# Kernel tuning notes

Hardware: AMD Instinct MI355X
Metric: run time of the kernel (lower is better)

Reference implementation:

```python
import jax, jax.numpy as jnp
import numpy as np

N_INP = 256
N_OUT = 16
H = 1024
UH = 32  # uni_hidden_unit
BATCH = 16384


def setup_inputs() -> dict:
    key = jax.random.key(0)
    ks = jax.random.split(key, 16)
    s = 0.02
    return {
        "x": jax.random.normal(ks[0], (BATCH, N_INP), dtype=jnp.float32),
        # main MLP: n_inp -> 1024 -> 1024 -> n_out
        "W0": jax.random.normal(ks[1], (N_INP, H), dtype=jnp.float32) * s,
        "b0": jnp.zeros((H,), jnp.float32),
        "W1": jax.random.normal(ks[2], (H, H), dtype=jnp.float32) * s,
        "b1": jnp.zeros((H,), jnp.float32),
        "W2": jax.random.normal(ks[3], (H, N_OUT), dtype=jnp.float32) * s,
        "b2": jnp.zeros((N_OUT,), jnp.float32),
        # stacked per-feature uni MLPs: 1 -> UH -> UH -> n_out, one per feature
        "uw1": jax.random.normal(ks[4], (N_INP, UH), dtype=jnp.float32) * s,
        "ub1": jnp.zeros((N_INP, UH), jnp.float32),
        "uw2": jax.random.normal(ks[5], (N_INP, UH, UH), dtype=jnp.float32) * s,
        "ub2": jnp.zeros((N_INP, UH), jnp.float32),
        "uw3": jax.random.normal(ks[6], (N_INP, UH, N_OUT), dtype=jnp.float32) * s,
        "ub3": jnp.zeros((N_INP, N_OUT), jnp.float32),
    }


def reference(x, W0, b0, W1, b1, W2, b2, uw1, ub1, uw2, ub2, uw3, ub3):
    # main MLP: Linear+ReLU, Linear+ReLU, Linear
    y = jax.nn.relu(x @ W0 + b0)
    y = jax.nn.relu(y @ W1 + b1)
    y = y @ W2 + b2  # [B, n_out]

    # per-feature univariate MLPs, vectorized over the feature axis i
    # input to uni MLP i is x[:, i:i+1]  -> first Linear(1, UH)
    h = jax.nn.relu(x[:, :, None] * uw1[None] + ub1[None])       # [B, I, UH]
    h = jax.nn.relu(jnp.einsum('bif,ifo->bio', h, uw2) + ub2[None])  # [B, I, UH]
    u = jnp.einsum('bif,ifo->bio', h, uw3) + ub3[None]           # [B, I, n_out]
    return y + u.sum(axis=1)
```

## Files before the change

kernel.cpp:

```cpp
#include <hip/hip_runtime.h>

typedef unsigned short u16;
typedef __attribute__((ext_vector_type(4))) float f32x4;
typedef __attribute__((ext_vector_type(4))) int i32x4;
typedef __attribute__((ext_vector_type(8))) __bf16 bf16x8;
typedef __attribute__((ext_vector_type(4))) unsigned short u16x4;

#define BATCH 16384
#define NINP 256
#define HID 1024
#define NOUT 16

__device__ __forceinline__ u16 f2bf(float f) {
  unsigned u = __builtin_bit_cast(unsigned, f);
  u += 0x7FFFu + ((u >> 16) & 1u);
  return (u16)(u >> 16);
}
__device__ __forceinline__ f32x4 mfma_bb(bf16x8 a, bf16x8 b, f32x4 c) {
  return __builtin_amdgcn_mfma_f32_16x16x32_bf16(a, b, c, 0, 0, 0);
}
__device__ __forceinline__ void gload_lds16(const void* g, void* l) {
  __builtin_amdgcn_global_load_lds(
      (const __attribute__((address_space(1))) void*)g,
      (__attribute__((address_space(3))) void*)l, 16, 0, 0);
}

static const size_t OFF_H0   = 0;
static const size_t OFF_PART = 0;
static const size_t OFF_H1   = 33554432;
static const size_t OFF_XB   = 33554432;
static const size_t OFF_W0T  = 67108864;
static const size_t OFF_W1T  = 67633152;
static const size_t OFF_W2T  = 69730304;
static const size_t OFF_UWP  = 69763072;
static const size_t OFF_CB   = 70811648;

__global__ __launch_bounds__(256) void k_prep(
    const float* __restrict__ x,
    const float* __restrict__ W0, const float* __restrict__ W1,
    const float* __restrict__ W2,
    const float* __restrict__ uw1, const float* __restrict__ ub1,
    const float* __restrict__ uw2, const float* __restrict__ ub2,
    const float* __restrict__ uw3, const float* __restrict__ b2,
    const float* __restrict__ ub3,
    u16* __restrict__ xb,
    u16* __restrict__ W0T, u16* __restrict__ W1T, u16* __restrict__ W2T,
    char* __restrict__ uwp, float* __restrict__ cb)
{
  __shared__ float tile[32][33];
  const int bid = blockIdx.x;
  const int tid = threadIdx.x;

  if (bid < 1312) {
    const float* src; u16* dst; int K, N, kb, ob;
    if (bid < 256)       { src = W0; dst = W0T; K = 256;  N = 1024; int t = bid;        kb = (t & 7) * 32;  ob = (t >> 3) * 32; }
    else if (bid < 1280) { src = W1; dst = W1T; K = 1024; N = 1024; int t = bid - 256;  kb = (t & 31) * 32; ob = (t >> 5) * 32; }
    else                 { src = W2; dst = W2T; K = 1024; N = 16;   int t = bid - 1280; kb = t * 32;        ob = 0; }
    const int tx = tid & 31, ty = tid >> 5;
    for (int r = ty; r < 32; r += 8)
      if (ob + tx < N) tile[r][tx] = src[(size_t)(kb + r) * N + ob + tx];
    __syncthreads();
    for (int r = ty; r < 32; r += 8)
      if (ob + r < N) dst[(size_t)(ob + r) * K + kb + tx] = f2bf(tile[tx][r]);
  } else if (bid < 5408) {
    const int idx = ((bid - 1312) * 256 + tid) * 4;
    const float4 v = *(const float4*)&x[idx];
    u16x4 o4 = { f2bf(v.x), f2bf(v.y), f2bf(v.z), f2bf(v.w) };
    *(u16x4*)&xb[idx] = o4;
  } else if (bid < 5664) {
    const int e = ((bid - 5408) * 256 + tid) * 4;
    const float4 v = *(const float4*)&uw2[e];
    const int i = e >> 10, f = (e >> 5) & 31, o = e & 31;
    const float vv[4] = { v.x, v.y, v.z, v.w };
    u16* blob16 = (u16*)(uwp + (size_t)i * 4096);
#pragma unroll
    for (int d = 0; d < 4; ++d) {
      const int oo = o + d;
      const int lane = ((f >> 3) << 4) | (oo & 15);
      blob16[256 + (oo >> 4) * 512 + lane * 8 + (f & 7)] = f2bf(vv[d]);
    }
  } else if (bid < 5792) {
    const int e = ((bid - 5664) * 256 + tid) * 4;
    const float4 v = *(const float4*)&uw3[e];
    const int i = e >> 9, f = (e >> 4) & 31, o2 = e & 15;
    const int s = (f < 16) ? (((f >> 2) << 3) + (f & 3))
                           : ((((f - 16) >> 2) << 3) + 4 + (f & 3));
    const float vv[4] = { v.x, v.y, v.z, v.w };
    u16* blob16 = (u16*)(uwp + (size_t)i * 4096);
#pragma unroll
    for (int d = 0; d < 4; ++d)
      blob16[1280 + ((s >> 3) * 16 + o2 + d) * 8 + (s & 7)] = f2bf(vv[d]);
  } else if (bid < 5816) {
    const int e4 = (bid - 5792) * 256 + tid;
    const int i = e4 / 24, r4 = e4 % 24;
    const float* src = (r4 < 8)  ? &uw1[i * 32 + r4 * 4]
                     : (r4 < 16) ? &ub1[i * 32 + (r4 - 8) * 4]
                                 : &ub2[i * 32 + (r4 - 16) * 4];
    *(float4*)(uwp + (size_t)i * 4096 + r4 * 16) = *(const float4*)src;
  } else {
    __shared__ float red[16][16];
    const int ig = tid >> 4, o = tid & 15;
    float s = 0.f;
#pragma unroll
    for (int k = 0; k < 16; ++k) s += ub3[(ig * 16 + k) * 16 + o];
    red[ig][o] = s;
    __syncthreads();
    if (tid < 16) {
      float t = b2[tid];
#pragma unroll
      for (int k = 0; k < 16; ++k) t += red[k][tid];
      cb[tid] = t;
    }
  }
}

__global__ __launch_bounds__(512, 2) void k_gemm8(
    const u16* __restrict__ A, const u16* __restrict__ BT,
    const float* __restrict__ bias, u16* __restrict__ C,
    int M, int N, int K)
{
  extern __shared__ __align__(16) char lds[];
  const int tid = threadIdx.x;
  const int lane = tid & 63, wid = tid >> 6;
  const int l15 = lane & 15, g = lane >> 4;
  const int wA = wid >> 2;
  const int wn = wid & 3;
  const int nbn = N >> 8;
  int logical = blockIdx.x;
  { const int nwg = gridDim.x;
    if ((nwg & 7) == 0) { const int q = nwg >> 3; logical = (logical & 7) * q + (logical >> 3); } }
  const int bm = logical / nbn, bn = logical - bm * nbn;
  const size_t rb = (size_t)bm * 256, cb = (size_t)bn * 256;

  const int q7 = l15 & 7;
  const int arow0 = wA * 128 + l15;
  const int brow0 = wn * 64 + l15;

  char* const ldsA = lds;
  char* const ldsB = lds + 65536;

  const u16* Ag = A + rb * K;
  const u16* Bg = BT + cb * K;

  f32x4 acc[8][4] = {};
  const int NT = K >> 6;

#define STAGE(arr, src, ktE, s) do { \
    const int G_ = (s) * 512 + tid; \
    const int row_ = G_ >> 3; \
    const int c8_ = (G_ & 7) ^ (row_ & 7); \
    gload_lds16(&(src)[(size_t)row_ * K + (ktE) + c8_ * 8], (arr) + G_ * 16); \
  } while (0)

#define ARD(bp, m, kk) (*(const bf16x8*)((bp) + (((arow0 + (m) * 16) * 8 + (((kk) * 4 + g) ^ q7)) << 4)))
#define BRD(bp, n, kk) (*(const bf16x8*)((bp) + (((brow0 + (n) * 16) * 8 + (((kk) * 4 + g) ^ q7)) << 4)))

#pragma unroll
  for (int s = 0; s < 4; ++s) STAGE(ldsA, Ag, 0, s);
#pragma unroll
  for (int s = 0; s < 4; ++s) STAGE(ldsB, Bg, 0, s);
  asm volatile("s_waitcnt vmcnt(0)" ::: "memory");
  __builtin_amdgcn_s_barrier();

  for (int t = 0; t < NT; ++t) {
    const int b = t & 1;
    const char* Ab = ldsA + b * 32768;
    const char* Bb = ldsB + b * 32768;
    char* An = ldsA + (b ^ 1) * 32768;
    char* Bn = ldsB + (b ^ 1) * 32768;
    const int kt1 = (t + 1) << 6;
    const bool stg = (t + 1 < NT);
    bf16x8 av[4][2], bv0[2][2], bv1[2][2];

#pragma unroll
    for (int m = 0; m < 4; ++m) { av[m][0] = ARD(Ab, m, 0); av[m][1] = ARD(Ab, m, 1); }
#pragma unroll
    for (int n = 0; n < 2; ++n) { bv0[n][0] = BRD(Bb, n, 0); bv0[n][1] = BRD(Bb, n, 1); }
    if (stg) { STAGE(An, Ag, kt1, 0); STAGE(Bn, Bg, kt1, 0); }
    __builtin_amdgcn_s_barrier();
    __builtin_amdgcn_s_setprio(1);
#pragma unroll
    for (int m = 0; m < 4; ++m)
#pragma unroll
      for (int n = 0; n < 2; ++n) {
        acc[m][n] = mfma_bb(av[m][0], bv0[n][0], acc[m][n]);
        acc[m][n] = mfma_bb(av[m][1], bv0[n][1], acc[m][n]);
      }
    __builtin_amdgcn_s_setprio(0);
    __builtin_amdgcn_s_barrier();

#pragma unroll
    for (int n = 0; n < 2; ++n) { bv1[n][0] = BRD(Bb, n + 2, 0); bv1[n][1] = BRD(Bb, n + 2, 1); }
    if (stg) { STAGE(An, Ag, kt1, 1); STAGE(Bn, Bg, kt1, 1); STAGE(An, Ag, kt1, 2); }
    __builtin_amdgcn_s_barrier();
    __builtin_amdgcn_s_setprio(1);
#pragma unroll
    for (int m = 0; m < 4; ++m)
#pragma unroll
      for (int n = 0; n < 2; ++n) {
        acc[m][n + 2] = mfma_bb(av[m][0], bv1[n][0], acc[m][n + 2]);
        acc[m][n + 2] = mfma_bb(av[m][1], bv1[n][1], acc[m][n + 2]);
      }
    __builtin_amdgcn_s_setprio(0);
    __builtin_amdgcn_s_barrier();

#pragma unroll
    for (int m = 0; m < 4; ++m) { av[m][0] = ARD(Ab, m + 4, 0); av[m][1] = ARD(Ab, m + 4, 1); }
    if (stg) { STAGE(Bn, Bg, kt1, 2); STAGE(An, Ag, kt1, 3); STAGE(Bn, Bg, kt1, 3); }
    __builtin_amdgcn_s_barrier();
    __builtin_amdgcn_s_setprio(1);
#pragma unroll
    for (int m = 0; m < 4; ++m)
#pragma unroll
      for (int n = 0; n < 2; ++n) {
        acc[m + 4][n + 2] = mfma_bb(av[m][0], bv1[n][0], acc[m + 4][n + 2]);
        acc[m + 4][n + 2] = mfma_bb(av[m][1], bv1[n][1], acc[m + 4][n + 2]);
      }
    __builtin_amdgcn_s_setprio(0);
    __builtin_amdgcn_s_barrier();

    __builtin_amdgcn_s_setprio(1);
#pragma unroll
    for (int m = 0; m < 4; ++m)
#pragma unroll
      for (int n = 0; n < 2; ++n) {
        acc[m + 4][n] = mfma_bb(av[m][0], bv0[n][0], acc[m + 4][n]);
        acc[m + 4][n] = mfma_bb(av[m][1], bv0[n][1], acc[m + 4][n]);
      }
    __builtin_amdgcn_s_setprio(0);
    asm volatile("s_waitcnt vmcnt(0)" ::: "memory");
    __builtin_amdgcn_s_barrier();
  }
#undef STAGE
#undef ARD
#undef BRD

  const int colb = (int)cb + wn * 64;
  const int rowb = (int)rb + wA * 128;
#pragma unroll
  for (int n = 0; n < 4; ++n) {
    const int col = colb + n * 16 + l15;
    const float bvs = bias[col];
#pragma unroll
    for (int m = 0; m < 8; ++m)
#pragma unroll
      for (int r = 0; r < 4; ++r) {
        const int row = rowb + m * 16 + g * 4 + r;
        C[(size_t)row * N + col] = f2bf(fmaxf(acc[m][n][r] + bvs, 0.f));
      }
  }
}

__global__ __launch_bounds__(256, 4) void k_uni(
    const float* __restrict__ x,
    const char* __restrict__ uwp,
    const u16* __restrict__ H1, const u16* __restrict__ W2T,
    float* __restrict__ part)
{
  const int tid = threadIdx.x, lane = tid & 63, wid = tid >> 6;
  const int l15 = lane & 15, g = lane >> 4;
  const int chunk = blockIdx.x & 7, rowblk = blockIdx.x >> 3;
  const int rb_blk = rowblk * 128;
  const int rb = rb_blk + wid * 32;
  const int i0 = chunk * 32;

  __shared__ __align__(16) float xt[128][33];
  __shared__ __align__(16) char wbuf[2][4096];

  {
    const int r0 = tid >> 3, c4 = (tid & 7) << 2;
#pragma unroll
    for (int rr = 0; rr < 128; rr += 32)
      *(float4*)&xt[rr + r0][c4] =
          *(const float4*)&x[(size_t)(rb_blk + rr + r0) * NINP + i0 + c4];
  }
  gload_lds16(uwp + (size_t)i0 * 4096 + tid * 16, &wbuf[0][tid * 16]);
  __syncthreads();

  const f32x4 zero4 = {0.f, 0.f, 0.f, 0.f};
  f32x4 acc0 = zero4, acc1 = zero4;
  const float* xr0 = &xt[wid * 32 + l15][0];
  const float* xr1 = &xt[wid * 32 + 16 + l15][0];

#pragma unroll 2
  for (int ii = 0; ii < 32; ++ii) {
    const int nxt = (ii + 1) & 31;
    gload_lds16(uwp + (size_t)(i0 + nxt) * 4096 + tid * 16,
                &wbuf[(ii + 1) & 1][tid * 16]);

    const char* bp = &wbuf[ii & 1][0];
    const f32x4 w1lo = *(const f32x4*)(bp + g * 32);
    const f32x4 w1hi = *(const f32x4*)(bp + g * 32 + 16);
    const f32x4 b1lo = *(const f32x4*)(bp + 128 + g * 32);
    const f32x4 b1hi = *(const f32x4*)(bp + 128 + g * 32 + 16);
    const f32x4 bb0  = *(const f32x4*)(bp + 256 + g * 16);
    const f32x4 bb1  = *(const f32x4*)(bp + 320 + g * 16);
    const bf16x8 bv0 = *(const bf16x8*)(bp + 512 + lane * 16);
    const bf16x8 bv1 = *(const bf16x8*)(bp + 1536 + lane * 16);
    const bf16x8 b3  = *(const bf16x8*)(bp + 2560 + lane * 16);
    const float xv0 = xr0[ii], xv1 = xr1[ii];

    bf16x8 af0, af1;
#pragma unroll
    for (int j = 0; j < 4; ++j) {
      af0[j]     = (__bf16)fmaxf(fmaf(xv0, w1lo[j], b1lo[j]), 0.f);
      af0[4 + j] = (__bf16)fmaxf(fmaf(xv0, w1hi[j], b1hi[j]), 0.f);
      af1[j]     = (__bf16)fmaxf(fmaf(xv1, w1lo[j], b1lo[j]), 0.f);
      af1[4 + j] = (__bf16)fmaxf(fmaf(xv1, w1hi[j], b1hi[j]), 0.f);
    }

    const f32x4 d00 = mfma_bb(bv0, af0, bb0);
    const f32x4 d10 = mfma_bb(bv1, af0, bb1);
    const f32x4 d01 = mfma_bb(bv0, af1, bb0);
    const f32x4 d11 = mfma_bb(bv1, af1, bb1);

    bf16x8 h20, h21;
#pragma unroll
    for (int j = 0; j < 4; ++j) {
      h20[j]     = (__bf16)fmaxf(d00[j], 0.f);
      h20[4 + j] = (__bf16)fmaxf(d10[j], 0.f);
      h21[j]     = (__bf16)fmaxf(d01[j], 0.f);
      h21[4 + j] = (__bf16)fmaxf(d11[j], 0.f);
    }

    acc0 = mfma_bb(b3, h20, acc0);
    acc1 = mfma_bb(b3, h21, acc1);

    __syncthreads();
  }

  {
    const int kb0 = chunk * 128;
#pragma unroll
    for (int kk = 0; kk < 4; ++kk) {
      const int kb = kb0 + kk * 32;
      const bf16x8 a0 = __builtin_bit_cast(bf16x8,
          *(const i32x4*)&H1[(size_t)(rb + l15) * HID + kb + g * 8]);
      const bf16x8 a1 = __builtin_bit_cast(bf16x8,
          *(const i32x4*)&H1[(size_t)(rb + 16 + l15) * HID + kb + g * 8]);
      const bf16x8 bv = __builtin_bit_cast(bf16x8,
          *(const i32x4*)&W2T[l15 * HID + kb + g * 8]);
      acc0 = mfma_bb(bv, a0, acc0);
      acc1 = mfma_bb(bv, a1, acc1);
    }
  }

  float* p = part + ((size_t)chunk * BATCH + rb) * NOUT;
  *(f32x4*)&p[l15 * 16 + g * 4] = acc0;
  *(f32x4*)&p[(16 + l15) * 16 + g * 4] = acc1;
}

__global__ __launch_bounds__(256) void k_reduce(
    const float* __restrict__ part, const float* __restrict__ cb,
    float* __restrict__ out)
{
  const int j4 = blockIdx.x * 256 + threadIdx.x;
  const float4 c = ((const float4*)cb)[j4 & 3];
  const float4* p = (const float4*)part;
  float rx = c.x, ry = c.y, rz = c.z, rw = c.w;
#pragma unroll
  for (int cc = 0; cc < 8; ++cc) {
    const float4 a = p[cc * 65536 + j4];
    rx += a.x; ry += a.y; rz += a.z; rw += a.w;
  }
  float4 r; r.x = rx; r.y = ry; r.z = rz; r.w = rw;
  ((float4*)out)[j4] = r;
}

extern "C" void kernel_launch(void* const* d_in, const int* in_sizes, int n_in,
                              void* d_out, int out_size, void* d_ws, size_t ws_size,
                              hipStream_t stream) {
  (void)in_sizes; (void)n_in; (void)out_size; (void)ws_size;
  const float* x   = (const float*)d_in[0];
  const float* W0  = (const float*)d_in[1];
  const float* b0  = (const float*)d_in[2];
  const float* W1  = (const float*)d_in[3];
  const float* b1  = (const float*)d_in[4];
  const float* W2  = (const float*)d_in[5];
  const float* b2  = (const float*)d_in[6];
  const float* uw1 = (const float*)d_in[7];
  const float* ub1 = (const float*)d_in[8];
  const float* uw2 = (const float*)d_in[9];
  const float* ub2 = (const float*)d_in[10];
  const float* uw3 = (const float*)d_in[11];
  const float* ub3 = (const float*)d_in[12];
  float* out = (float*)d_out;

  char* ws = (char*)d_ws;
  u16*   H0   = (u16*)(ws + OFF_H0);
  u16*   H1   = (u16*)(ws + OFF_H1);
  u16*   xb   = (u16*)(ws + OFF_XB);
  u16*   W0T  = (u16*)(ws + OFF_W0T);
  u16*   W1T  = (u16*)(ws + OFF_W1T);
  u16*   W2T  = (u16*)(ws + OFF_W2T);
  char*  uwp  = (char*)(ws + OFF_UWP);
  float* cb   = (float*)(ws + OFF_CB);
  float* part = (float*)(ws + OFF_PART);

  hipFuncSetAttribute((const void*)k_gemm8,
                      hipFuncAttributeMaxDynamicSharedMemorySize, 131072);

  k_prep<<<5817, 256, 0, stream>>>(x, W0, W1, W2, uw1, ub1, uw2, ub2, uw3,
                                   b2, ub3, xb, W0T, W1T, W2T, uwp, cb);
  k_gemm8<<<256, 512, 131072, stream>>>(xb, W0T, b0, H0, BATCH, HID, NINP);
  k_gemm8<<<256, 512, 131072, stream>>>(H0, W1T, b1, H1, BATCH, HID, HID);
  k_uni<<<1024, 256, 0, stream>>>(x, uwp, H1, W2T, part);
  k_reduce<<<256, 256, 0, stream>>>(part, cb, out);
}
```

Baseline: 109.8 us.

## Stage GEMM epilogue through swizzled LDS for 16-byte coalesced stores; rebalance prefetch

```diff
diff --git a/kernel.cpp b/kernel.cpp
--- a/kernel.cpp
+++ b/kernel.cpp
@@ -176,7 +176,7 @@
     for (int m = 0; m < 4; ++m) { av[m][0] = ARD(Ab, m, 0); av[m][1] = ARD(Ab, m, 1); }
 #pragma unroll
     for (int n = 0; n < 2; ++n) { bv0[n][0] = BRD(Bb, n, 0); bv0[n][1] = BRD(Bb, n, 1); }
-    if (stg) { STAGE(An, Ag, kt1, 0); STAGE(Bn, Bg, kt1, 0); }
+    if (stg) { STAGE(An, Ag, kt1, 0); STAGE(Bn, Bg, kt1, 0); STAGE(An, Ag, kt1, 1); STAGE(Bn, Bg, kt1, 1); }
     __builtin_amdgcn_s_barrier();
     __builtin_amdgcn_s_setprio(1);
 #pragma unroll
@@ -191,7 +191,7 @@
 
 #pragma unroll
     for (int n = 0; n < 2; ++n) { bv1[n][0] = BRD(Bb, n + 2, 0); bv1[n][1] = BRD(Bb, n + 2, 1); }
-    if (stg) { STAGE(An, Ag, kt1, 1); STAGE(Bn, Bg, kt1, 1); STAGE(An, Ag, kt1, 2); }
+    if (stg) { STAGE(An, Ag, kt1, 2); STAGE(Bn, Bg, kt1, 2); STAGE(An, Ag, kt1, 3); STAGE(Bn, Bg, kt1, 3); }
     __builtin_amdgcn_s_barrier();
     __builtin_amdgcn_s_setprio(1);
 #pragma unroll
@@ -206,7 +206,6 @@
 
 #pragma unroll
     for (int m = 0; m < 4; ++m) { av[m][0] = ARD(Ab, m + 4, 0); av[m][1] = ARD(Ab, m + 4, 1); }
-    if (stg) { STAGE(Bn, Bg, kt1, 2); STAGE(An, Ag, kt1, 3); STAGE(Bn, Bg, kt1, 3); }
     __builtin_amdgcn_s_barrier();
     __builtin_amdgcn_s_setprio(1);
 #pragma unroll
@@ -235,19 +234,36 @@
 #undef ARD
 #undef BRD
 
-  const int colb = (int)cb + wn * 64;
-  const int rowb = (int)rb + wA * 128;
-#pragma unroll
-  for (int n = 0; n < 4; ++n) {
-    const int col = colb + n * 16 + l15;
-    const float bvs = bias[col];
-#pragma unroll
-    for (int m = 0; m < 8; ++m)
-#pragma unroll
-      for (int r = 0; r < 4; ++r) {
-        const int row = rowb + m * 16 + g * 4 + r;
-        C[(size_t)row * N + col] = f2bf(fmaxf(acc[m][n][r] + bvs, 0.f));
+  {
+    char* const ep = lds;
+    float bv[4];
+#pragma unroll
+    for (int n = 0; n < 4; ++n) bv[n] = bias[cb + wn * 64 + n * 16 + l15];
+#pragma unroll
+    for (int h = 0; h < 2; ++h) {
+      __syncthreads();
+#pragma unroll
+      for (int mloc = 0; mloc < 4; ++mloc)
+#pragma unroll
+        for (int n = 0; n < 4; ++n) {
+          const int col = wn * 64 + n * 16 + l15;
+#pragma unroll
+          for (int r = 0; r < 4; ++r) {
+            const int lrow = wA * 64 + mloc * 16 + g * 4 + r;
+            *(u16*)(ep + lrow * 512 + ((col * 2) ^ ((lrow & 7) << 4))) =
+                f2bf(fmaxf(acc[h * 4 + mloc][n][r] + bv[n], 0.f));
+          }
+        }
+      __syncthreads();
+#pragma unroll
+      for (int p = 0; p < 8; ++p) {
+        const int ci = p * 512 + tid;
+        const int lrow = ci >> 5, c16 = ci & 31;
+        const i32x4 v = *(const i32x4*)(ep + lrow * 512 + ((c16 * 16) ^ ((lrow & 7) << 4)));
+        const int grow = (int)rb + (lrow >> 6) * 128 + h * 64 + (lrow & 63);
+        *(i32x4*)&C[(size_t)grow * N + cb + c16 * 8] = v;
       }
+    }
   }
 }
 
```

New measurement: 102.1 us. 1.08x faster.
